# Optimization experiments

Measured on AMD Instinct MI355X. Metric: run time of the kernel, lower is better.

Reference implementation:

```python
import jax, jax.numpy as jnp
import numpy as np

N = 4096          # num_nodes
F = 64            # node_features
H = 128           # hidden_dim
NH = 4            # num_heads
HD = H // NH      # per-head dim = 32
L = 3             # num_layers
C = 7             # num_classes
EDGE_P = 0.004    # ~16 avg degree


def setup_inputs() -> dict:
    key = jax.random.key(0)
    ks = jax.random.split(key, 20)
    g = lambda k, shape, fan_in: jax.random.normal(k, shape, jnp.float32) / np.sqrt(fan_in)
    x = jax.random.normal(ks[0], (N, F), jnp.float32)
    adj = (jax.random.uniform(ks[1], (N, N)) < EDGE_P).astype(jnp.float32)
    return {
        "x": x,
        "adj": adj,
        "enc_W": g(ks[2], (F, H), F), "enc_b": jnp.zeros((H,), jnp.float32),
        "gcn_W": g(ks[3], (L, H, H), H), "gcn_b": jnp.zeros((L, H), jnp.float32),
        "attn_W": g(ks[4], (L, NH, H, HD), H), "attn_Wb": jnp.zeros((L, NH, HD), jnp.float32),
        "attn_a": g(ks[5], (L, NH, 2 * HD), 2 * HD), "attn_ab": jnp.zeros((L, NH), jnp.float32),
        "cls_W1": g(ks[6], (H, H // 2), H), "cls_b1": jnp.zeros((H // 2,), jnp.float32),
        "cls_W2": g(ks[7], (H // 2, C), H // 2), "cls_b2": jnp.zeros((C,), jnp.float32),
        "con_W1": g(ks[8], (H, H // 2), H), "con_b1": jnp.zeros((H // 2,), jnp.float32),
        "con_W2": g(ks[9], (H // 2, 1), H // 2), "con_b2": jnp.zeros((1,), jnp.float32),
    }


def _normalize_adj(adj):
    a = adj + jnp.eye(adj.shape[0], dtype=adj.dtype)
    dinv = jnp.sum(a, axis=1) ** -0.5
    return dinv[:, None] * a * dinv[None, :]


def _gcn(h, adj_norm, W, b):
    support = adj_norm @ h                      # [N,H]
    return jax.nn.relu(support @ W + b)         # dropout=0 (eval)


def _attention(h, edge_mask, W, Wb, a, ab):
    # h:[N,H], W:[NH,H,HD], a:[NH,2*HD]; per-pair score = Linear(concat(h_i,h_j))
    hh = jnp.einsum('nf,hfd->hnd', h, W) + Wb[:, None, :]     # [NH,N,HD]
    a_src, a_dst = a[:, :HD], a[:, HD:]
    s_src = jnp.einsum('hnd,hd->hn', hh, a_src)               # [NH,N]
    s_dst = jnp.einsum('hnd,hd->hn', hh, a_dst)               # [NH,N]
    scores = s_src[:, :, None] + s_dst[:, None, :] + ab[:, None, None]
    # original uses literal 0.0 (NOT -inf) for non-edges before softmax
    scores = jnp.where(edge_mask[None, :, :], scores, 0.0)    # [NH,N,N]
    probs = jax.nn.softmax(scores, axis=-1)
    out = jnp.einsum('hij,hjd->hid', probs, hh)               # [NH,N,HD]
    return out.transpose(1, 0, 2).reshape(h.shape[0], NH * HD)


def reference(x, adj, enc_W, enc_b, gcn_W, gcn_b, attn_W, attn_Wb, attn_a, attn_ab,
              cls_W1, cls_b1, cls_W2, cls_b2, con_W1, con_b1, con_W2, con_b2):
    h = jax.nn.relu(x @ enc_W + enc_b)          # node encoder (dropout=0)
    adj_norm = _normalize_adj(adj)
    edge_mask = adj > 0
    for i in range(L):
        h_gcn = _gcn(h, adj_norm, gcn_W[i], gcn_b[i])
        h_attn = _attention(h, edge_mask, attn_W[i], attn_Wb[i], attn_a[i], attn_ab[i])
        h = jax.nn.relu(h_gcn + h_attn)
    node_logits = jax.nn.relu(h @ cls_W1 + cls_b1) @ cls_W2 + cls_b2
    h_mean = jnp.mean(h, axis=0, keepdims=True)
    contagion = jax.nn.relu(h_mean @ con_W1 + con_b1) @ con_W2 + con_b2
    return (node_logits, h, contagion)
```

## Files before the change

### kernel.cpp

```cpp
#include <hip/hip_runtime.h>

typedef unsigned short u16;

#define N 4096
#define F 64
#define H 128
#define NH 4
#define HD 32
#define EMAX 64
#define RB 2

__device__ float2 g_pkA[N * H];
__device__ float2 g_pkB[N * H];
__device__ u16   g_cols[N * EMAX];
__device__ int   g_deg[N];
__device__ float g_dinv[N];
__device__ float g_ssrcA[N * NH];
__device__ float g_ssrcB[N * NH];
__device__ float g_sdstA[N * NH];
__device__ float g_sdstB[N * NH];
__device__ float g_zr[(3 * 32 + 32) * H];

__device__ __forceinline__ void agg2(int i0, int tid, const float2* __restrict__ pk,
                                     const float* __restrict__ ssrc_in,
                                     const float* __restrict__ sdst_in,
                                     const float* __restrict__ part,
                                     const float* __restrict__ abv,
                                     int (&jl)[RB][EMAX], float (&dv)[RB][EMAX],
                                     float (&wl)[RB][EMAX * NH],
                                     float& outa, float& sup) {
  int c = tid & 127, rg = tid >> 7, hc = c >> 5;
#pragma unroll
  for (int r = 0; r < RB; ++r) {
    int dd = g_deg[i0 + r];
    const u16* cl = g_cols + (size_t)(i0 + r) * EMAX;
    for (int e = tid; e < dd; e += 256) {
      int j = cl[e];
      jl[r][e] = j;
      dv[r][e] = g_dinv[j];
    }
  }
  __syncthreads();

  int lg = tid & 31;
  int i = i0 + rg, dd = g_deg[i];
  float em, S, base;
  {
    float s0 = -INFINITY, s1 = -INFINITY;
    if (lg < dd)      s0 = sdst_in[jl[rg][lg] * NH + hc];
    if (lg + 32 < dd) s1 = sdst_in[jl[rg][lg + 32] * NH + hc];
    float M = fmaxf(s0, s1);
#pragma unroll
    for (int m = 16; m >= 1; m >>= 1) M = fmaxf(M, __shfl_xor(M, m, 64));
    float ssrc = ssrc_in[i * NH + hc];
    float ab = abv[hc];
    float mv = fmaxf(0.f, ssrc + ab + M);
    em = expf(-mv);
    base = ssrc + ab - mv;
    float Sp = 0.f;
    if (lg < dd) {
      float w0 = expf(base + s0);
      wl[rg][lg * NH + hc] = w0;
      Sp = w0;
    }
    if (lg + 32 < dd) {
      float w1 = expf(base + s1);
      wl[rg][(lg + 32) * NH + hc] = w1;
      Sp += w1;
    }
#pragma unroll
    for (int m = 16; m >= 1; m >>= 1) Sp += __shfl_xor(Sp, m, 64);
    S = Sp;
  }
  __syncthreads();

  float sumc = 0.f;
#pragma unroll
  for (int s = 0; s < 32; ++s) sumc += part[s * H + c];

  const float2* pkc = pk + c;
  float aA = 0.f, aT = 0.f, aG = 0.f;
  int e = 0;
  for (; e + 4 <= dd; e += 4) {
    int j0 = jl[rg][e],     j1 = jl[rg][e + 1];
    int j2 = jl[rg][e + 2], j3 = jl[rg][e + 3];
    float2 q0 = pkc[j0 * H], q1 = pkc[j1 * H];
    float2 q2 = pkc[j2 * H], q3 = pkc[j3 * H];
    float w0 = wl[rg][e * NH + hc],       w1 = wl[rg][(e + 1) * NH + hc];
    float w2 = wl[rg][(e + 2) * NH + hc], w3 = wl[rg][(e + 3) * NH + hc];
    aA = fmaf(w0, q0.y, aA); aA = fmaf(w1, q1.y, aA);
    aA = fmaf(w2, q2.y, aA); aA = fmaf(w3, q3.y, aA);
    aT += (q0.y + q1.y) + (q2.y + q3.y);
    aG = fmaf(dv[rg][e], q0.x, aG);     aG = fmaf(dv[rg][e + 1], q1.x, aG);
    aG = fmaf(dv[rg][e + 2], q2.x, aG); aG = fmaf(dv[rg][e + 3], q3.x, aG);
  }
  for (; e < dd; ++e) {
    int j = jl[rg][e];
    float2 q = pkc[j * H];
    float w = wl[rg][e * NH + hc];
    aA = fmaf(w, q.y, aA);
    aT += q.y;
    aG = fmaf(dv[rg][e], q.x, aG);
  }
  float Z = S + em * (float)(N - dd);
  outa = (aA + em * (sumc - aT)) / Z;
  float di = g_dinv[i];
  sup = di * (aG + di * pkc[i * H].x);
}

__device__ __forceinline__ void proj2(int i0, int tid, const float (&hrowT)[H][RB],
                                      const float* __restrict__ aW,
                                      const float* __restrict__ aWb,
                                      const float* __restrict__ aa,
                                      float* __restrict__ part, float hval,
                                      float2* __restrict__ pkout,
                                      float* __restrict__ ssrc_out,
                                      float* __restrict__ sdst_out) {
  int c = tid & 127, rg = tid >> 7, hc = c >> 5, dc = c & 31;
  float p = aWb[hc * HD + dc];
  for (int f = 0; f < H; ++f)
    p = fmaf(hrowT[f][rg], aW[(hc * H + f) * HD + dc], p);
  int r = i0 + rg;
  pkout[r * H + c] = make_float2(hval, p);
  const float* ap = aa + hc * 2 * HD;
  float ss = p * ap[dc], sd = p * ap[HD + dc];
#pragma unroll
  for (int m = 16; m >= 1; m >>= 1) {
    ss += __shfl_xor(ss, m, 64);
    sd += __shfl_xor(sd, m, 64);
  }
  if (dc == 0) {
    ssrc_out[r * NH + hc] = ss;
    sdst_out[r * NH + hc] = sd;
  }
  atomicAdd(&part[(r & 31) * H + c], p);
}

__global__ void k_csr_enc(const float* __restrict__ adj, const float* __restrict__ x,
                          const float* __restrict__ eW, const float* __restrict__ eb,
                          const float* __restrict__ aW, const float* __restrict__ aWb,
                          const float* __restrict__ aa) {
  __shared__ float xT[F][RB];
  __shared__ float hrowT[H][RB];
  __shared__ int cnt;
  int tid = threadIdx.x;
  if (blockIdx.x < N / RB) {
    int i0 = blockIdx.x * RB;
    int c = tid & 127, rg = tid >> 7;
    if (tid < F * RB) {
      int r = tid >> 6, k = tid & 63;
      xT[k][r] = x[(i0 + r) * F + k];
    }
    __syncthreads();
    float e = eb[c];
    for (int k = 0; k < F; ++k)
      e = fmaf(xT[k][rg], eW[k * H + c], e);
    e = fmaxf(e, 0.f);
    hrowT[c][rg] = e;
    __syncthreads();
    proj2(i0, tid, hrowT, aW, aWb, aa, g_zr, e, g_pkA, g_ssrcA, g_sdstA);
  } else {
    int row = blockIdx.x - N / RB;
    if (tid == 0) cnt = 0;
    __syncthreads();
    const float* rp = adj + (size_t)row * N;
    float4 q[4];
#pragma unroll
    for (int k2 = 0; k2 < 4; ++k2)
      q[k2] = *reinterpret_cast<const float4*>(rp + k2 * 1024 + tid * 4);
#pragma unroll
    for (int k2 = 0; k2 < 4; ++k2) {
      int base = k2 * 1024 + tid * 4;
      float v[4] = {q[k2].x, q[k2].y, q[k2].z, q[k2].w};
#pragma unroll
      for (int t = 0; t < 4; ++t)
        if (v[t] != 0.f) {
          int pos = atomicAdd(&cnt, 1);
          if (pos < EMAX) g_cols[row * EMAX + pos] = (u16)(base + t);
        }
    }
    __syncthreads();
    if (tid == 0) {
      g_deg[row] = cnt < EMAX ? cnt : EMAX;
      g_dinv[row] = 1.0f / sqrtf((float)(cnt + 1));
    }
  }
}

__global__ void k_acp(int pp, int l, const float* __restrict__ gW,
                      const float* __restrict__ gb, const float* __restrict__ aW,
                      const float* __restrict__ aWb, const float* __restrict__ aa,
                      const float* __restrict__ abv) {
  const float2* pk    = pp ? g_pkB : g_pkA;
  float2*       pkout = pp ? g_pkA : g_pkB;
  const float*  ssin  = pp ? g_ssrcB : g_ssrcA;
  float*        ssout = pp ? g_ssrcA : g_ssrcB;
  const float*  sdin  = pp ? g_sdstB : g_sdstA;
  float*        sdout = pp ? g_sdstA : g_sdstB;
  __shared__ int   jl[RB][EMAX];
  __shared__ float dv[RB][EMAX];
  __shared__ float wl[RB][EMAX * NH];
  __shared__ float srowT[H][RB];
  __shared__ float hrowT[H][RB];
  int i0 = blockIdx.x * RB, tid = threadIdx.x;
  int c = tid & 127, rg = tid >> 7;

  float oa, sp;
  agg2(i0, tid, pk, ssin, sdin, g_zr + l * 32 * H, abv, jl, dv, wl, oa, sp);
  srowT[c][rg] = sp;
  __syncthreads();

  float a = gb[c];
  for (int f = 0; f < H; ++f)
    a = fmaf(srowT[f][rg], gW[f * H + c], a);
  float g = fmaxf(fmaxf(a, 0.f) + oa, 0.f);
  hrowT[c][rg] = g;
  __syncthreads();

  proj2(i0, tid, hrowT, aW, aWb, aa, g_zr + (l + 1) * 32 * H, g,
        pkout, ssout, sdout);
}

__global__ void k_acc(const float* __restrict__ abv, const float* __restrict__ gW,
                      const float* __restrict__ gb,
                      const float* __restrict__ W1, const float* __restrict__ b1,
                      const float* __restrict__ W2, const float* __restrict__ b2,
                      float* __restrict__ out, float* __restrict__ outh) {
  __shared__ int   jl[RB][EMAX];
  __shared__ float dv[RB][EMAX];
  __shared__ float wl[RB][EMAX * NH];
  __shared__ float srowT[H][RB];
  __shared__ float hrowT[H][RB];
  __shared__ float tl[RB][64];
  int i0 = blockIdx.x * RB, tid = threadIdx.x;
  int c = tid & 127, rg = tid >> 7;

  float oa, sp;
  agg2(i0, tid, g_pkA, g_ssrcA, g_sdstA, g_zr + 2 * 32 * H, abv, jl, dv, wl, oa, sp);
  srowT[c][rg] = sp;
  __syncthreads();

  float a = gb[c];
  for (int f = 0; f < H; ++f)
    a = fmaf(srowT[f][rg], gW[f * H + c], a);
  float g = fmaxf(fmaxf(a, 0.f) + oa, 0.f);
  int r = i0 + rg;
  outh[r * H + c] = g;
  hrowT[c][rg] = g;
  atomicAdd(&g_zr[(3 * 32 + (r & 31)) * H + c], g);
  __syncthreads();

  if (tid < 128) {
    int rr = tid >> 6, u = tid & 63;
    float a2 = b1[u];
    for (int f = 0; f < H; ++f)
      a2 = fmaf(hrowT[f][rr], W1[f * 64 + u], a2);
    tl[rr][u] = fmaxf(a2, 0.f);
  }
  __syncthreads();
  if (tid < 7 * RB) {
    int rr = tid / 7, j = tid - rr * 7;
    float p = b2[j];
    for (int v = 0; v < 64; ++v)
      p = fmaf(tl[rr][v], W2[v * 7 + j], p);
    out[(i0 + rr) * 7 + j] = p;
  }
}

__global__ void k_contagion(const float* __restrict__ W1, const float* __restrict__ b1,
                            const float* __restrict__ W2, const float* __restrict__ b2,
                            float* __restrict__ out) {
  __shared__ float hm[H];
  __shared__ float tl[64];
  int u = threadIdx.x;
  const float* hp = g_zr + 3 * 32 * H;
#pragma unroll
  for (int q = 0; q < 2; ++q) {
    int col = u + q * 64;
    float s = 0.f;
#pragma unroll
    for (int sl = 0; sl < 32; ++sl) s += hp[sl * H + col];
    hm[col] = s * (1.0f / 4096.0f);
  }
  __syncthreads();
  float acc = b1[u];
  for (int f = 0; f < H; ++f) acc = fmaf(hm[f], W1[f * 64 + u], acc);
  tl[u] = fmaxf(acc, 0.f);
  __syncthreads();
  if (u == 0) {
    float p = b2[0];
    for (int v = 0; v < 64; ++v) p = fmaf(tl[v], W2[v], p);
    out[0] = p;
  }
}

extern "C" void kernel_launch(void* const* d_in, const int* in_sizes, int n_in,
                              void* d_out, int out_size, void* d_ws, size_t ws_size,
                              hipStream_t stream) {
  const float* x       = (const float*)d_in[0];
  const float* adj     = (const float*)d_in[1];
  const float* enc_W   = (const float*)d_in[2];
  const float* enc_b   = (const float*)d_in[3];
  const float* gcn_W   = (const float*)d_in[4];
  const float* gcn_b   = (const float*)d_in[5];
  const float* attn_W  = (const float*)d_in[6];
  const float* attn_Wb = (const float*)d_in[7];
  const float* attn_a  = (const float*)d_in[8];
  const float* attn_ab = (const float*)d_in[9];
  const float* cls_W1  = (const float*)d_in[10];
  const float* cls_b1  = (const float*)d_in[11];
  const float* cls_W2  = (const float*)d_in[12];
  const float* cls_b2  = (const float*)d_in[13];
  const float* con_W1  = (const float*)d_in[14];
  const float* con_b1  = (const float*)d_in[15];
  const float* con_W2  = (const float*)d_in[16];
  const float* con_b2  = (const float*)d_in[17];
  (void)in_sizes; (void)n_in; (void)d_ws; (void)ws_size; (void)out_size;

  float* out = (float*)d_out;
  float* outh = out + (size_t)N * 7;
  float* outc = out + (size_t)N * 7 + (size_t)N * H;

  void* zr = nullptr;
  hipGetSymbolAddress(&zr, HIP_SYMBOL(g_zr));
  hipMemsetAsync(zr, 0, sizeof(float) * (3 * 32 + 32) * H, stream);

  k_csr_enc<<<N / RB + N, 256, 0, stream>>>(adj, x, enc_W, enc_b,
                                            attn_W, attn_Wb, attn_a);
  k_acp<<<N / RB, 256, 0, stream>>>(0, 0, gcn_W, gcn_b,
                                    attn_W + (size_t)1 * NH * H * HD,
                                    attn_Wb + (size_t)1 * NH * HD,
                                    attn_a + (size_t)1 * NH * 2 * HD, attn_ab);
  k_acp<<<N / RB, 256, 0, stream>>>(1, 1, gcn_W + (size_t)1 * H * H, gcn_b + H,
                                    attn_W + (size_t)2 * NH * H * HD,
                                    attn_Wb + (size_t)2 * NH * HD,
                                    attn_a + (size_t)2 * NH * 2 * HD, attn_ab + NH);
  k_acc<<<N / RB, 256, 0, stream>>>(attn_ab + 2 * NH, gcn_W + (size_t)2 * H * H,
                                    gcn_b + 2 * H, cls_W1, cls_b1, cls_W2, cls_b2,
                                    out, outh);
  k_contagion<<<1, 64, 0, stream>>>(con_W1, con_b1, con_W2, con_b2, outc);
}
```

Baseline: 244.4 us.

## Split fused layer kernel into aggregation and 8-row dense projection kernels

Each fused aggregate-plus-projection layer kernel becomes two kernels. One does the sparse gather over 2 rows per block and writes the attention and GCN partial results to global buffers. The other does the dense GCN and attention projections over 8 rows per block, reusing every weight load across 4 rows per thread. Column-sum partials shrink from 32 strided slots to one atomic per block, and the encoder and classifier also move to 8-row tiles. This cuts redundant weight traffic and the per-row serial FMA chains, at the cost of extra kernel launches and an N×H intermediate round trip through global memory.

```diff
diff --git a/kernel.cpp b/kernel.cpp
--- a/kernel.cpp
+++ b/kernel.cpp
@@ -8,7 +8,8 @@
 #define NH 4
 #define HD 32
 #define EMAX 64
-#define RB 2
+#define RA 2
+#define RW 8
 
 __device__ float2 g_pkA[N * H];
 __device__ float2 g_pkB[N * H];
@@ -19,19 +20,125 @@
 __device__ float g_ssrcB[N * NH];
 __device__ float g_sdstA[N * NH];
 __device__ float g_sdstB[N * NH];
-__device__ float g_zr[(3 * 32 + 32) * H];
-
-__device__ __forceinline__ void agg2(int i0, int tid, const float2* __restrict__ pk,
-                                     const float* __restrict__ ssrc_in,
-                                     const float* __restrict__ sdst_in,
-                                     const float* __restrict__ part,
-                                     const float* __restrict__ abv,
-                                     int (&jl)[RB][EMAX], float (&dv)[RB][EMAX],
-                                     float (&wl)[RB][EMAX * NH],
-                                     float& outa, float& sup) {
+__device__ float g_sp[N * H];
+__device__ float g_oa[N * H];
+__device__ float g_zr[4 * H];
+
+__global__ __launch_bounds__(256) void k_csr_enc(
+    const float* __restrict__ adj, const float* __restrict__ x,
+    const float* __restrict__ eW, const float* __restrict__ eb,
+    const float* __restrict__ aW, const float* __restrict__ aWb,
+    const float* __restrict__ aa) {
+  __shared__ float sT[RW][132];
+  __shared__ float csum[H];
+  __shared__ int cnt;
+  int tid = threadIdx.x;
+  if (blockIdx.x < N / RW) {
+    int i0 = blockIdx.x * RW;
+    if (tid < 128) {
+      int r = tid >> 4, ch = tid & 15;
+      float4 v = *reinterpret_cast<const float4*>(x + (size_t)(i0 + r) * F + ch * 4);
+      *reinterpret_cast<float4*>(&sT[r][ch * 4]) = v;
+    }
+    __syncthreads();
+    int c = tid & 127, rg = tid >> 7, hc = c >> 5, dc = c & 31;
+    float e0 = eb[c];
+    float acc[4] = {e0, e0, e0, e0};
+    for (int f = 0; f < F; f += 4) {
+      float w0 = eW[(f + 0) * H + c], w1 = eW[(f + 1) * H + c];
+      float w2 = eW[(f + 2) * H + c], w3 = eW[(f + 3) * H + c];
+#pragma unroll
+      for (int k = 0; k < 4; ++k) {
+        float4 xv = *reinterpret_cast<const float4*>(&sT[rg * 4 + k][f]);
+        acc[k] = fmaf(xv.x, w0, acc[k]); acc[k] = fmaf(xv.y, w1, acc[k]);
+        acc[k] = fmaf(xv.z, w2, acc[k]); acc[k] = fmaf(xv.w, w3, acc[k]);
+      }
+    }
+    float g[4];
+#pragma unroll
+    for (int k = 0; k < 4; ++k) g[k] = fmaxf(acc[k], 0.f);
+    __syncthreads();
+#pragma unroll
+    for (int k = 0; k < 4; ++k) sT[rg * 4 + k][c] = g[k];
+    __syncthreads();
+    float pb = aWb[hc * HD + dc];
+    float p[4] = {pb, pb, pb, pb};
+    const float* aWh = aW + (size_t)hc * H * HD + dc;
+    for (int f = 0; f < H; f += 4) {
+      float w0 = aWh[(f + 0) * HD], w1 = aWh[(f + 1) * HD];
+      float w2 = aWh[(f + 2) * HD], w3 = aWh[(f + 3) * HD];
+#pragma unroll
+      for (int k = 0; k < 4; ++k) {
+        float4 gv = *reinterpret_cast<const float4*>(&sT[rg * 4 + k][f]);
+        p[k] = fmaf(gv.x, w0, p[k]); p[k] = fmaf(gv.y, w1, p[k]);
+        p[k] = fmaf(gv.z, w2, p[k]); p[k] = fmaf(gv.w, w3, p[k]);
+      }
+    }
+    const float* ap = aa + hc * 2 * HD;
+    float as = ap[dc], ad = ap[HD + dc];
+#pragma unroll
+    for (int k = 0; k < 4; ++k) {
+      float ss = p[k] * as, sd = p[k] * ad;
+#pragma unroll
+      for (int m = 16; m >= 1; m >>= 1) {
+        ss += __shfl_xor(ss, m, 64);
+        sd += __shfl_xor(sd, m, 64);
+      }
+      if (dc == 0) {
+        int r = i0 + rg * 4 + k;
+        g_ssrcA[r * NH + hc] = ss;
+        g_sdstA[r * NH + hc] = sd;
+      }
+    }
+    float psum = (p[0] + p[1]) + (p[2] + p[3]);
+#pragma unroll
+    for (int k = 0; k < 4; ++k) {
+      int r = i0 + rg * 4 + k;
+      g_pkA[(size_t)r * H + c] = make_float2(g[k], p[k]);
+    }
+    if (rg == 0) csum[c] = psum;
+    __syncthreads();
+    if (rg == 1) atomicAdd(&g_zr[c], csum[c] + psum);
+  } else {
+    int row = blockIdx.x - N / RW;
+    if (tid == 0) cnt = 0;
+    __syncthreads();
+    const float* rp = adj + (size_t)row * N;
+    float4 q[4];
+#pragma unroll
+    for (int k2 = 0; k2 < 4; ++k2)
+      q[k2] = *reinterpret_cast<const float4*>(rp + k2 * 1024 + tid * 4);
+#pragma unroll
+    for (int k2 = 0; k2 < 4; ++k2) {
+      int base = k2 * 1024 + tid * 4;
+      float v[4] = {q[k2].x, q[k2].y, q[k2].z, q[k2].w};
+#pragma unroll
+      for (int t = 0; t < 4; ++t)
+        if (v[t] != 0.f) {
+          int pos = atomicAdd(&cnt, 1);
+          if (pos < EMAX) g_cols[row * EMAX + pos] = (u16)(base + t);
+        }
+    }
+    __syncthreads();
+    if (tid == 0) {
+      g_deg[row] = cnt < EMAX ? cnt : EMAX;
+      g_dinv[row] = 1.0f / sqrtf((float)(cnt + 1));
+    }
+  }
+}
+
+__global__ __launch_bounds__(256) void k_agg(int pp, int l,
+                                             const float* __restrict__ abv) {
+  const float2* pk  = pp ? g_pkB : g_pkA;
+  const float* ssin = pp ? g_ssrcB : g_ssrcA;
+  const float* sdin = pp ? g_sdstB : g_sdstA;
+  __shared__ int   jl[RA][EMAX];
+  __shared__ float dv[RA][EMAX];
+  __shared__ float wl[RA][EMAX * NH];
+  int i0 = blockIdx.x * RA, tid = threadIdx.x;
   int c = tid & 127, rg = tid >> 7, hc = c >> 5;
 #pragma unroll
-  for (int r = 0; r < RB; ++r) {
+  for (int r = 0; r < RA; ++r) {
     int dd = g_deg[i0 + r];
     const u16* cl = g_cols + (size_t)(i0 + r) * EMAX;
     for (int e = tid; e < dd; e += 256) {
@@ -47,12 +154,12 @@
   float em, S, base;
   {
     float s0 = -INFINITY, s1 = -INFINITY;
-    if (lg < dd)      s0 = sdst_in[jl[rg][lg] * NH + hc];
-    if (lg + 32 < dd) s1 = sdst_in[jl[rg][lg + 32] * NH + hc];
+    if (lg < dd)      s0 = sdin[jl[rg][lg] * NH + hc];
+    if (lg + 32 < dd) s1 = sdin[jl[rg][lg + 32] * NH + hc];
     float M = fmaxf(s0, s1);
 #pragma unroll
     for (int m = 16; m >= 1; m >>= 1) M = fmaxf(M, __shfl_xor(M, m, 64));
-    float ssrc = ssrc_in[i * NH + hc];
+    float ssrc = ssin[i * NH + hc];
     float ab = abv[hc];
     float mv = fmaxf(0.f, ssrc + ab + M);
     em = expf(-mv);
@@ -74,9 +181,7 @@
   }
   __syncthreads();
 
-  float sumc = 0.f;
-#pragma unroll
-  for (int s = 0; s < 32; ++s) sumc += part[s * H + c];
+  float sumc = g_zr[l * H + c];
 
   const float2* pkc = pk + c;
   float aA = 0.f, aT = 0.f, aG = 0.f;
@@ -84,8 +189,8 @@
   for (; e + 4 <= dd; e += 4) {
     int j0 = jl[rg][e],     j1 = jl[rg][e + 1];
     int j2 = jl[rg][e + 2], j3 = jl[rg][e + 3];
-    float2 q0 = pkc[j0 * H], q1 = pkc[j1 * H];
-    float2 q2 = pkc[j2 * H], q3 = pkc[j3 * H];
+    float2 q0 = pkc[(size_t)j0 * H], q1 = pkc[(size_t)j1 * H];
+    float2 q2 = pkc[(size_t)j2 * H], q3 = pkc[(size_t)j3 * H];
     float w0 = wl[rg][e * NH + hc],       w1 = wl[rg][(e + 1) * NH + hc];
     float w2 = wl[rg][(e + 2) * NH + hc], w3 = wl[rg][(e + 3) * NH + hc];
     aA = fmaf(w0, q0.y, aA); aA = fmaf(w1, q1.y, aA);
@@ -96,174 +201,161 @@
   }
   for (; e < dd; ++e) {
     int j = jl[rg][e];
-    float2 q = pkc[j * H];
+    float2 q = pkc[(size_t)j * H];
     float w = wl[rg][e * NH + hc];
     aA = fmaf(w, q.y, aA);
     aT += q.y;
     aG = fmaf(dv[rg][e], q.x, aG);
   }
   float Z = S + em * (float)(N - dd);
-  outa = (aA + em * (sumc - aT)) / Z;
   float di = g_dinv[i];
-  sup = di * (aG + di * pkc[i * H].x);
-}
-
-__device__ __forceinline__ void proj2(int i0, int tid, const float (&hrowT)[H][RB],
-                                      const float* __restrict__ aW,
-                                      const float* __restrict__ aWb,
-                                      const float* __restrict__ aa,
-                                      float* __restrict__ part, float hval,
-                                      float2* __restrict__ pkout,
-                                      float* __restrict__ ssrc_out,
-                                      float* __restrict__ sdst_out) {
+  g_oa[(size_t)i * H + c] = (aA + em * (sumc - aT)) / Z;
+  g_sp[(size_t)i * H + c] = di * (aG + di * pkc[(size_t)i * H].x);
+}
+
+__global__ __launch_bounds__(256) void k_dense(
+    int outB, int lsum, const float* __restrict__ gW, const float* __restrict__ gb,
+    const float* __restrict__ aW, const float* __restrict__ aWb,
+    const float* __restrict__ aa) {
+  float2* pkout = outB ? g_pkB : g_pkA;
+  float* ssout  = outB ? g_ssrcB : g_ssrcA;
+  float* sdout  = outB ? g_sdstB : g_sdstA;
+  __shared__ float sT[RW][132];
+  __shared__ float csum[H];
+  int i0 = blockIdx.x * RW, tid = threadIdx.x;
+  {
+    int r = tid >> 5, ch = tid & 31;
+    float4 v = *reinterpret_cast<const float4*>(g_sp + (size_t)(i0 + r) * H + ch * 4);
+    *reinterpret_cast<float4*>(&sT[r][ch * 4]) = v;
+  }
+  __syncthreads();
   int c = tid & 127, rg = tid >> 7, hc = c >> 5, dc = c & 31;
-  float p = aWb[hc * HD + dc];
-  for (int f = 0; f < H; ++f)
-    p = fmaf(hrowT[f][rg], aW[(hc * H + f) * HD + dc], p);
-  int r = i0 + rg;
-  pkout[r * H + c] = make_float2(hval, p);
+  float b0 = gb[c];
+  float a[4] = {b0, b0, b0, b0};
+  for (int f = 0; f < H; f += 4) {
+    float w0 = gW[(f + 0) * H + c], w1 = gW[(f + 1) * H + c];
+    float w2 = gW[(f + 2) * H + c], w3 = gW[(f + 3) * H + c];
+#pragma unroll
+    for (int k = 0; k < 4; ++k) {
+      float4 sv = *reinterpret_cast<const float4*>(&sT[rg * 4 + k][f]);
+      a[k] = fmaf(sv.x, w0, a[k]); a[k] = fmaf(sv.y, w1, a[k]);
+      a[k] = fmaf(sv.z, w2, a[k]); a[k] = fmaf(sv.w, w3, a[k]);
+    }
+  }
+  float g[4];
+#pragma unroll
+  for (int k = 0; k < 4; ++k) {
+    int r = i0 + rg * 4 + k;
+    float o = g_oa[(size_t)r * H + c];
+    g[k] = fmaxf(fmaxf(a[k], 0.f) + o, 0.f);
+  }
+  __syncthreads();
+#pragma unroll
+  for (int k = 0; k < 4; ++k) sT[rg * 4 + k][c] = g[k];
+  __syncthreads();
+  float pb = aWb[hc * HD + dc];
+  float p[4] = {pb, pb, pb, pb};
+  const float* aWh = aW + (size_t)hc * H * HD + dc;
+  for (int f = 0; f < H; f += 4) {
+    float w0 = aWh[(f + 0) * HD], w1 = aWh[(f + 1) * HD];
+    float w2 = aWh[(f + 2) * HD], w3 = aWh[(f + 3) * HD];
+#pragma unroll
+    for (int k = 0; k < 4; ++k) {
+      float4 gv = *reinterpret_cast<const float4*>(&sT[rg * 4 + k][f]);
+      p[k] = fmaf(gv.x, w0, p[k]); p[k] = fmaf(gv.y, w1, p[k]);
+      p[k] = fmaf(gv.z, w2, p[k]); p[k] = fmaf(gv.w, w3, p[k]);
+    }
+  }
   const float* ap = aa + hc * 2 * HD;
-  float ss = p * ap[dc], sd = p * ap[HD + dc];
-#pragma unroll
-  for (int m = 16; m >= 1; m >>= 1) {
-    ss += __shfl_xor(ss, m, 64);
-    sd += __shfl_xor(sd, m, 64);
-  }
-  if (dc == 0) {
-    ssrc_out[r * NH + hc] = ss;
-    sdst_out[r * NH + hc] = sd;
-  }
-  atomicAdd(&part[(r & 31) * H + c], p);
-}
-
-__global__ void k_csr_enc(const float* __restrict__ adj, const float* __restrict__ x,
-                          const float* __restrict__ eW, const float* __restrict__ eb,
-                          const float* __restrict__ aW, const float* __restrict__ aWb,
-                          const float* __restrict__ aa) {
-  __shared__ float xT[F][RB];
-  __shared__ float hrowT[H][RB];
-  __shared__ int cnt;
-  int tid = threadIdx.x;
-  if (blockIdx.x < N / RB) {
-    int i0 = blockIdx.x * RB;
-    int c = tid & 127, rg = tid >> 7;
-    if (tid < F * RB) {
-      int r = tid >> 6, k = tid & 63;
-      xT[k][r] = x[(i0 + r) * F + k];
-    }
-    __syncthreads();
-    float e = eb[c];
-    for (int k = 0; k < F; ++k)
-      e = fmaf(xT[k][rg], eW[k * H + c], e);
-    e = fmaxf(e, 0.f);
-    hrowT[c][rg] = e;
-    __syncthreads();
-    proj2(i0, tid, hrowT, aW, aWb, aa, g_zr, e, g_pkA, g_ssrcA, g_sdstA);
-  } else {
-    int row = blockIdx.x - N / RB;
-    if (tid == 0) cnt = 0;
-    __syncthreads();
-    const float* rp = adj + (size_t)row * N;
-    float4 q[4];
-#pragma unroll
-    for (int k2 = 0; k2 < 4; ++k2)
-      q[k2] = *reinterpret_cast<const float4*>(rp + k2 * 1024 + tid * 4);
-#pragma unroll
-    for (int k2 = 0; k2 < 4; ++k2) {
-      int base = k2 * 1024 + tid * 4;
-      float v[4] = {q[k2].x, q[k2].y, q[k2].z, q[k2].w};
-#pragma unroll
-      for (int t = 0; t < 4; ++t)
-        if (v[t] != 0.f) {
-          int pos = atomicAdd(&cnt, 1);
-          if (pos < EMAX) g_cols[row * EMAX + pos] = (u16)(base + t);
-        }
-    }
-    __syncthreads();
-    if (tid == 0) {
-      g_deg[row] = cnt < EMAX ? cnt : EMAX;
-      g_dinv[row] = 1.0f / sqrtf((float)(cnt + 1));
-    }
-  }
-}
-
-__global__ void k_acp(int pp, int l, const float* __restrict__ gW,
-                      const float* __restrict__ gb, const float* __restrict__ aW,
-                      const float* __restrict__ aWb, const float* __restrict__ aa,
-                      const float* __restrict__ abv) {
-  const float2* pk    = pp ? g_pkB : g_pkA;
-  float2*       pkout = pp ? g_pkA : g_pkB;
-  const float*  ssin  = pp ? g_ssrcB : g_ssrcA;
-  float*        ssout = pp ? g_ssrcA : g_ssrcB;
-  const float*  sdin  = pp ? g_sdstB : g_sdstA;
-  float*        sdout = pp ? g_sdstA : g_sdstB;
-  __shared__ int   jl[RB][EMAX];
-  __shared__ float dv[RB][EMAX];
-  __shared__ float wl[RB][EMAX * NH];
-  __shared__ float srowT[H][RB];
-  __shared__ float hrowT[H][RB];
-  int i0 = blockIdx.x * RB, tid = threadIdx.x;
+  float as = ap[dc], ad = ap[HD + dc];
+#pragma unroll
+  for (int k = 0; k < 4; ++k) {
+    float ss = p[k] * as, sd = p[k] * ad;
+#pragma unroll
+    for (int m = 16; m >= 1; m >>= 1) {
+      ss += __shfl_xor(ss, m, 64);
+      sd += __shfl_xor(sd, m, 64);
+    }
+    if (dc == 0) {
+      int r = i0 + rg * 4 + k;
+      ssout[r * NH + hc] = ss;
+      sdout[r * NH + hc] = sd;
+    }
+  }
+  float psum = (p[0] + p[1]) + (p[2] + p[3]);
+#pragma unroll
+  for (int k = 0; k < 4; ++k) {
+    int r = i0 + rg * 4 + k;
+    pkout[(size_t)r * H + c] = make_float2(g[k], p[k]);
+  }
+  if (rg == 0) csum[c] = psum;
+  __syncthreads();
+  if (rg == 1) atomicAdd(&g_zr[lsum * H + c], csum[c] + psum);
+}
+
+__global__ __launch_bounds__(256) void k_dcls(
+    const float* __restrict__ gW, const float* __restrict__ gb,
+    const float* __restrict__ W1, const float* __restrict__ b1,
+    const float* __restrict__ W2, const float* __restrict__ b2,
+    float* __restrict__ out, float* __restrict__ outh) {
+  __shared__ float sT[RW][132];
+  __shared__ float csum[H];
+  __shared__ float zl[RW][65];
+  int i0 = blockIdx.x * RW, tid = threadIdx.x;
+  {
+    int r = tid >> 5, ch = tid & 31;
+    float4 v = *reinterpret_cast<const float4*>(g_sp + (size_t)(i0 + r) * H + ch * 4);
+    *reinterpret_cast<float4*>(&sT[r][ch * 4]) = v;
+  }
+  __syncthreads();
   int c = tid & 127, rg = tid >> 7;
-
-  float oa, sp;
-  agg2(i0, tid, pk, ssin, sdin, g_zr + l * 32 * H, abv, jl, dv, wl, oa, sp);
-  srowT[c][rg] = sp;
-  __syncthreads();
-
-  float a = gb[c];
-  for (int f = 0; f < H; ++f)
-    a = fmaf(srowT[f][rg], gW[f * H + c], a);
-  float g = fmaxf(fmaxf(a, 0.f) + oa, 0.f);
-  hrowT[c][rg] = g;
-  __syncthreads();
-
-  proj2(i0, tid, hrowT, aW, aWb, aa, g_zr + (l + 1) * 32 * H, g,
-        pkout, ssout, sdout);
-}
-
-__global__ void k_acc(const float* __restrict__ abv, const float* __restrict__ gW,
-                      const float* __restrict__ gb,
-                      const float* __restrict__ W1, const float* __restrict__ b1,
-                      const float* __restrict__ W2, const float* __restrict__ b2,
-                      float* __restrict__ out, float* __restrict__ outh) {
-  __shared__ int   jl[RB][EMAX];
-  __shared__ float dv[RB][EMAX];
-  __shared__ float wl[RB][EMAX * NH];
-  __shared__ float srowT[H][RB];
-  __shared__ float hrowT[H][RB];
-  __shared__ float tl[RB][64];
-  int i0 = blockIdx.x * RB, tid = threadIdx.x;
-  int c = tid & 127, rg = tid >> 7;
-
-  float oa, sp;
-  agg2(i0, tid, g_pkA, g_ssrcA, g_sdstA, g_zr + 2 * 32 * H, abv, jl, dv, wl, oa, sp);
-  srowT[c][rg] = sp;
-  __syncthreads();
-
-  float a = gb[c];
-  for (int f = 0; f < H; ++f)
-    a = fmaf(srowT[f][rg], gW[f * H + c], a);
-  float g = fmaxf(fmaxf(a, 0.f) + oa, 0.f);
-  int r = i0 + rg;
-  outh[r * H + c] = g;
-  hrowT[c][rg] = g;
-  atomicAdd(&g_zr[(3 * 32 + (r & 31)) * H + c], g);
-  __syncthreads();
-
-  if (tid < 128) {
-    int rr = tid >> 6, u = tid & 63;
-    float a2 = b1[u];
-    for (int f = 0; f < H; ++f)
-      a2 = fmaf(hrowT[f][rr], W1[f * 64 + u], a2);
-    tl[rr][u] = fmaxf(a2, 0.f);
-  }
-  __syncthreads();
-  if (tid < 7 * RB) {
+  float b0 = gb[c];
+  float a[4] = {b0, b0, b0, b0};
+  for (int f = 0; f < H; f += 4) {
+    float w0 = gW[(f + 0) * H + c], w1 = gW[(f + 1) * H + c];
+    float w2 = gW[(f + 2) * H + c], w3 = gW[(f + 3) * H + c];
+#pragma unroll
+    for (int k = 0; k < 4; ++k) {
+      float4 sv = *reinterpret_cast<const float4*>(&sT[rg * 4 + k][f]);
+      a[k] = fmaf(sv.x, w0, a[k]); a[k] = fmaf(sv.y, w1, a[k]);
+      a[k] = fmaf(sv.z, w2, a[k]); a[k] = fmaf(sv.w, w3, a[k]);
+    }
+  }
+  float g[4];
+#pragma unroll
+  for (int k = 0; k < 4; ++k) {
+    int r = i0 + rg * 4 + k;
+    float o = g_oa[(size_t)r * H + c];
+    g[k] = fmaxf(fmaxf(a[k], 0.f) + o, 0.f);
+    outh[(size_t)r * H + c] = g[k];
+  }
+  __syncthreads();
+  float gsum = (g[0] + g[1]) + (g[2] + g[3]);
+#pragma unroll
+  for (int k = 0; k < 4; ++k) sT[rg * 4 + k][c] = g[k];
+  if (rg == 0) csum[c] = gsum;
+  __syncthreads();
+  if (rg == 1) atomicAdd(&g_zr[3 * H + c], csum[c] + gsum);
+  int u = tid & 63, rq = tid >> 6;
+  float z[2] = {b1[u], b1[u]};
+  for (int f = 0; f < H; f += 4) {
+    float w0 = W1[(f + 0) * 64 + u], w1 = W1[(f + 1) * 64 + u];
+    float w2 = W1[(f + 2) * 64 + u], w3 = W1[(f + 3) * 64 + u];
+#pragma unroll
+    for (int k2 = 0; k2 < 2; ++k2) {
+      float4 gv = *reinterpret_cast<const float4*>(&sT[rq * 2 + k2][f]);
+      z[k2] = fmaf(gv.x, w0, z[k2]); z[k2] = fmaf(gv.y, w1, z[k2]);
+      z[k2] = fmaf(gv.z, w2, z[k2]); z[k2] = fmaf(gv.w, w3, z[k2]);
+    }
+  }
+#pragma unroll
+  for (int k2 = 0; k2 < 2; ++k2) zl[rq * 2 + k2][u] = fmaxf(z[k2], 0.f);
+  __syncthreads();
+  if (tid < RW * 7) {
     int rr = tid / 7, j = tid - rr * 7;
-    float p = b2[j];
-    for (int v = 0; v < 64; ++v)
-      p = fmaf(tl[rr][v], W2[v * 7 + j], p);
-    out[(i0 + rr) * 7 + j] = p;
+    float pv = b2[j];
+    for (int v = 0; v < 64; ++v) pv = fmaf(zl[rr][v], W2[v * 7 + j], pv);
+    out[(size_t)(i0 + rr) * 7 + j] = pv;
   }
 }
 
@@ -273,15 +365,8 @@
   __shared__ float hm[H];
   __shared__ float tl[64];
   int u = threadIdx.x;
-  const float* hp = g_zr + 3 * 32 * H;
-#pragma unroll
-  for (int q = 0; q < 2; ++q) {
-    int col = u + q * 64;
-    float s = 0.f;
-#pragma unroll
-    for (int sl = 0; sl < 32; ++sl) s += hp[sl * H + col];
-    hm[col] = s * (1.0f / 4096.0f);
-  }
+  hm[u]      = g_zr[3 * H + u]      * (1.0f / 4096.0f);
+  hm[u + 64] = g_zr[3 * H + u + 64] * (1.0f / 4096.0f);
   __syncthreads();
   float acc = b1[u];
   for (int f = 0; f < H; ++f) acc = fmaf(hm[f], W1[f * 64 + u], acc);
@@ -323,20 +408,22 @@
 
   void* zr = nullptr;
   hipGetSymbolAddress(&zr, HIP_SYMBOL(g_zr));
-  hipMemsetAsync(zr, 0, sizeof(float) * (3 * 32 + 32) * H, stream);
-
-  k_csr_enc<<<N / RB + N, 256, 0, stream>>>(adj, x, enc_W, enc_b,
+  hipMemsetAsync(zr, 0, sizeof(float) * 4 * H, stream);
+
+  k_csr_enc<<<N / RW + N, 256, 0, stream>>>(adj, x, enc_W, enc_b,
                                             attn_W, attn_Wb, attn_a);
-  k_acp<<<N / RB, 256, 0, stream>>>(0, 0, gcn_W, gcn_b,
-                                    attn_W + (size_t)1 * NH * H * HD,
-                                    attn_Wb + (size_t)1 * NH * HD,
-                                    attn_a + (size_t)1 * NH * 2 * HD, attn_ab);
-  k_acp<<<N / RB, 256, 0, stream>>>(1, 1, gcn_W + (size_t)1 * H * H, gcn_b + H,
-                                    attn_W + (size_t)2 * NH * H * HD,
-                                    attn_Wb + (size_t)2 * NH * HD,
-                                    attn_a + (size_t)2 * NH * 2 * HD, attn_ab + NH);
-  k_acc<<<N / RB, 256, 0, stream>>>(attn_ab + 2 * NH, gcn_W + (size_t)2 * H * H,
-                                    gcn_b + 2 * H, cls_W1, cls_b1, cls_W2, cls_b2,
-                                    out, outh);
+  k_agg<<<N / RA, 256, 0, stream>>>(0, 0, attn_ab);
+  k_dense<<<N / RW, 256, 0, stream>>>(1, 1, gcn_W, gcn_b,
+                                      attn_W + (size_t)1 * NH * H * HD,
+                                      attn_Wb + (size_t)1 * NH * HD,
+                                      attn_a + (size_t)1 * NH * 2 * HD);
+  k_agg<<<N / RA, 256, 0, stream>>>(1, 1, attn_ab + NH);
+  k_dense<<<N / RW, 256, 0, stream>>>(0, 2, gcn_W + (size_t)1 * H * H, gcn_b + H,
+                                      attn_W + (size_t)2 * NH * H * HD,
+                                      attn_Wb + (size_t)2 * NH * HD,
+                                      attn_a + (size_t)2 * NH * 2 * HD);
+  k_agg<<<N / RA, 256, 0, stream>>>(0, 2, attn_ab + 2 * NH);
+  k_dcls<<<N / RW, 256, 0, stream>>>(gcn_W + (size_t)2 * H * H, gcn_b + 2 * H,
+                                     cls_W1, cls_b1, cls_W2, cls_b2, out, outh);
   k_contagion<<<1, 64, 0, stream>>>(con_W1, con_b1, con_W2, con_b2, outc);
 }
```

Measured after the change: 324.6 us. +32.9%, slower.
